# Optimization experiments

Hardware: AMD Instinct MI355X
Metric: run time of the kernel (lower is better)

The kernel has to match this reference:

```python
import jax, jax.numpy as jnp
import numpy as np

N = 50000
E = 800000
IN_DIM = 128
HID = 128
OUT = 40


def setup_inputs() -> dict:
    key = jax.random.key(0)
    k1, k2, k3, k4, k5 = jax.random.split(key, 5)
    x = jax.random.normal(k1, (N, IN_DIM), dtype=jnp.float32)
    edge_index = jax.random.randint(k2, (2, E), 0, N, dtype=jnp.int64)
    # Glorot-ish init for GCNConv weights, zero bias (PyG default bias=True)
    W1 = jax.random.normal(k3, (IN_DIM, HID), dtype=jnp.float32) / np.sqrt(IN_DIM)
    b1 = jnp.zeros((HID,), dtype=jnp.float32)
    W2 = jax.random.normal(k4, (HID, OUT), dtype=jnp.float32) / np.sqrt(HID)
    b2 = jnp.zeros((OUT,), dtype=jnp.float32)
    return {"x": x, "edge_index": edge_index, "W1": W1, "b1": b1, "W2": W2, "b2": b2}


def _gcn_norm(edge_index, n_nodes):
    """Add self-loops and compute symmetric GCN normalization per edge.
    Returns (src, dst, norm) with len E + n_nodes."""
    loops = jnp.arange(n_nodes, dtype=edge_index.dtype)
    src = jnp.concatenate([edge_index[0], loops])
    dst = jnpp_concat = jnp.concatenate([edge_index[1], loops])
    dst = jnp.concatenate([edge_index[1], loops])
    deg = jax.ops.segment_sum(jnp.ones_like(dst, dtype=jnp.float32), dst,
                              num_segments=n_nodes)
    dinv = jnp.where(deg > 0, jax.lax.rsqrt(deg), 0.0)
    norm = dinv[src] * dinv[dst]  # [E + N]
    return src, dst, norm


def _gcn_conv(x, src, dst, norm, W, b, n_nodes):
    xw = x @ W                                  # [N, F_out] transform first
    msg = xw[src] * norm[:, None]               # gather + scale, [E+N, F_out]
    out = jax.ops.segment_sum(msg, dst, num_segments=n_nodes)  # scatter-add
    return out + b


def reference(x, edge_index, W1, b1, W2, b2):
    n = x.shape[0]
    src, dst, norm = _gcn_norm(edge_index, n)
    h = _gcn_conv(x, src, dst, norm, W1, b1, n)
    h = jax.nn.relu(h)
    # dropout is identity in eval mode (training=False)
    h = _gcn_conv(h, src, dst, norm, W2, b2, n)
    return jax.nn.softmax(h, axis=1)
```

## Files before the change

### kernel.cpp

```cpp
#include <hip/hip_runtime.h>
#include <hip/hip_fp16.h>

#define IN_DIM 128
#define HID    128
#define OUTC   40
#define CAP    64
#define LSTR   136
#define NBS    1024
#define NBG1   256

typedef _Float16 f16x8 __attribute__((ext_vector_type(8)));
typedef _Float16 f16x4 __attribute__((ext_vector_type(4)));
typedef float    f32x4 __attribute__((ext_vector_type(4)));
typedef int      i32x4 __attribute__((ext_vector_type(4)));

__device__ __forceinline__ int permi(int d, int NP8) { return (d & 7) * NP8 + (d >> 3); }

__device__ __forceinline__ f16x8 cvt8(f32x4 lo, f32x4 hi) {
  f16x8 r;
  r[0] = (_Float16)lo[0]; r[1] = (_Float16)lo[1]; r[2] = (_Float16)lo[2]; r[3] = (_Float16)lo[3];
  r[4] = (_Float16)hi[0]; r[5] = (_Float16)hi[1]; r[6] = (_Float16)hi[2]; r[7] = (_Float16)hi[3];
  return r;
}

__global__ __launch_bounds__(256) void k_scatter_gemm1(const int* __restrict__ edge, int* __restrict__ cnt,
                                                       unsigned short* __restrict__ col,
                                                       const float* __restrict__ x, const float* __restrict__ W1,
                                                       __half* __restrict__ xws,
                                                       int E, int n, int NP8, int nT) {
  __shared__ _Float16 sW[128 * 128];
  int b   = blockIdx.x;
  int c40 = b / 40, r40 = b % 40;
  int tid = threadIdx.x;
  int E4  = E >> 2;

  if (r40 < 32) {
    int g = b & 7;
    auto proc = [&](int d, int s) {
      if ((d & 7) != g || (unsigned)d >= (unsigned)n || (unsigned)s >= (unsigned)n) return;
      int p   = g * NP8 + (d >> 3);
      int pos = atomicAdd(&cnt[p], 1);
      if (pos < CAP) col[(size_t)p * CAP + pos] = (unsigned short)s;
    };
    int j = c40 * 4 + (r40 >> 3);
    int t = j * 256 + tid;
    const int gstride = (NBS >> 3) * 256;
    const i32x4* srcv = (const i32x4*)edge;
    const i32x4* dstv = (const i32x4*)&edge[E];
    for (int q = t; q < E4; q += gstride) {
      i32x4 dq = __builtin_nontemporal_load(&dstv[q]);
      i32x4 sq = __builtin_nontemporal_load(&srcv[q]);
      proc(dq[0], sq[0]); proc(dq[1], sq[1]); proc(dq[2], sq[2]); proc(dq[3], sq[3]);
    }
    if (b == 0) {
      for (int e = E4 * 4 + tid; e < E; e += 256) {
        int d  = edge[E + e];
        int sv = edge[e];
        if ((unsigned)d >= (unsigned)n || (unsigned)sv >= (unsigned)n) continue;
        int p   = (d & 7) * NP8 + (d >> 3);
        int pos = atomicAdd(&cnt[p], 1);
        if (pos < CAP) col[(size_t)p * CAP + pos] = (unsigned short)sv;
      }
    }
    return;
  }

  {
    const f32x4* w4 = (const f32x4*)W1;
    for (int idx = tid; idx < 4096; idx += 256) {
      int kk = idx >> 5, nn4 = (idx & 31) * 4;
      f32x4 v = w4[idx];
#pragma unroll
      for (int j = 0; j < 4; ++j) {
        int nn = nn4 + j;
        sW[nn * 128 + (kk ^ ((nn & 7) << 3))] = (_Float16)v[j];
      }
    }
  }
  __syncthreads();
  int wv = tid >> 6, lane = tid & 63, m = lane & 15, quad = lane >> 4;
  int sw = (m & 7) << 3;
  int bg = c40 * 8 + (r40 - 32);
  for (int tile = bg; tile < nT; tile += NBG1) {
    int i0   = tile * 64;
    int arow = i0 + 16 * wv + m;
    f16x8 a0, a1, a2, a3;
    if (arow < n) {
      const float* xr = &x[(size_t)arow * IN_DIM + quad * 8];
      f32x4 u0 = __builtin_nontemporal_load((const f32x4*)(xr));
      f32x4 u1 = __builtin_nontemporal_load((const f32x4*)(xr + 4));
      f32x4 u2 = __builtin_nontemporal_load((const f32x4*)(xr + 32));
      f32x4 u3 = __builtin_nontemporal_load((const f32x4*)(xr + 36));
      f32x4 u4 = __builtin_nontemporal_load((const f32x4*)(xr + 64));
      f32x4 u5 = __builtin_nontemporal_load((const f32x4*)(xr + 68));
      f32x4 u6 = __builtin_nontemporal_load((const f32x4*)(xr + 96));
      f32x4 u7 = __builtin_nontemporal_load((const f32x4*)(xr + 100));
      a0 = cvt8(u0, u1); a1 = cvt8(u2, u3); a2 = cvt8(u4, u5); a3 = cvt8(u6, u7);
    } else {
#pragma unroll
      for (int jj = 0; jj < 8; ++jj) {
        a0[jj] = (_Float16)0.f; a1[jj] = (_Float16)0.f; a2[jj] = (_Float16)0.f; a3[jj] = (_Float16)0.f;
      }
    }
    int base_row = i0 + 16 * wv + quad * 4;
#pragma unroll
    for (int t = 0; t < 8; ++t) {
      const _Float16* bx = &sW[(t * 16 + m) * 128];
      f16x8 bf0 = *(const f16x8*)&bx[(quad * 8 +  0) ^ sw];
      f16x8 bf1 = *(const f16x8*)&bx[(quad * 8 + 32) ^ sw];
      f16x8 bf2 = *(const f16x8*)&bx[(quad * 8 + 64) ^ sw];
      f16x8 bf3 = *(const f16x8*)&bx[(quad * 8 + 96) ^ sw];
      f32x4 c = {0.f, 0.f, 0.f, 0.f};
      c = __builtin_amdgcn_mfma_f32_16x16x32_f16(a0, bf0, c, 0, 0, 0);
      c = __builtin_amdgcn_mfma_f32_16x16x32_f16(a1, bf1, c, 0, 0, 0);
      c = __builtin_amdgcn_mfma_f32_16x16x32_f16(a2, bf2, c, 0, 0, 0);
      c = __builtin_amdgcn_mfma_f32_16x16x32_f16(a3, bf3, c, 0, 0, 0);
      int colb = t * 16 + m;
#pragma unroll
      for (int r = 0; r < 4; ++r) {
        int row = base_row + r;
        if (row < n) xws[(size_t)row * HID + colb] = __float2half(c[r]);
      }
    }
  }
}

__global__ __launch_bounds__(256) void k_agg1(const uint2* __restrict__ xws2, const int* __restrict__ cnt,
                                              const unsigned short* __restrict__ col, const float* __restrict__ b1,
                                              uint2* __restrict__ hv, int n, int NP8) {
  int wvid = (blockIdx.x * 256 + threadIdx.x) >> 6;
  int lane = threadIdx.x & 63;
  int half = lane >> 5;
  int f    = lane & 31;
  int wid  = wvid * 2 + half;
  if (wid >= n) return;
  int p   = permi(wid, NP8);
  int deg = cnt[p];
  float dvd = rsqrtf((float)(deg + 1));
  uint2 sv = xws2[(size_t)wid * 32 + f];
  float2 slo = __half22float2(*(__half2*)&sv.x);
  float2 shi = __half22float2(*(__half2*)&sv.y);
  float ax = slo.x * dvd, ay = slo.y * dvd, az = shi.x * dvd, aw = shi.y * dvd;
  int end = min(deg, CAP);
  const unsigned short* cp = &col[(size_t)p * CAP];
  int e = 0;
  for (; e + 4 <= end; e += 4) {
    uint2 cw = *(const uint2*)&cp[e];
    int s0 = cw.x & 0xffff, s1 = cw.x >> 16;
    int s2 = cw.y & 0xffff, s3 = cw.y >> 16;
    float d0 = rsqrtf((float)(cnt[permi(s0, NP8)] + 1));
    float d1 = rsqrtf((float)(cnt[permi(s1, NP8)] + 1));
    float d2 = rsqrtf((float)(cnt[permi(s2, NP8)] + 1));
    float d3 = rsqrtf((float)(cnt[permi(s3, NP8)] + 1));
    uint2 v0 = xws2[(size_t)s0 * 32 + f];
    uint2 v1 = xws2[(size_t)s1 * 32 + f];
    uint2 v2 = xws2[(size_t)s2 * 32 + f];
    uint2 v3 = xws2[(size_t)s3 * 32 + f];
    float2 l0 = __half22float2(*(__half2*)&v0.x), h0 = __half22float2(*(__half2*)&v0.y);
    float2 l1 = __half22float2(*(__half2*)&v1.x), h1 = __half22float2(*(__half2*)&v1.y);
    float2 l2 = __half22float2(*(__half2*)&v2.x), h2 = __half22float2(*(__half2*)&v2.y);
    float2 l3 = __half22float2(*(__half2*)&v3.x), h3 = __half22float2(*(__half2*)&v3.y);
    ax += l0.x * d0 + l1.x * d1 + l2.x * d2 + l3.x * d3;
    ay += l0.y * d0 + l1.y * d1 + l2.y * d2 + l3.y * d3;
    az += h0.x * d0 + h1.x * d1 + h2.x * d2 + h3.x * d3;
    aw += h0.y * d0 + h1.y * d1 + h2.y * d2 + h3.y * d3;
  }
  for (; e < end; ++e) {
    int s    = cp[e];
    float dv = rsqrtf((float)(cnt[permi(s, NP8)] + 1));
    uint2 v  = xws2[(size_t)s * 32 + f];
    float2 l = __half22float2(*(__half2*)&v.x), hh = __half22float2(*(__half2*)&v.y);
    ax += l.x * dv; ay += l.y * dv; az += hh.x * dv; aw += hh.y * dv;
  }
  float4 bb = ((const float4*)b1)[f];
  __half2 o0 = __floats2half2_rn(fmaxf(ax * dvd + bb.x, 0.f), fmaxf(ay * dvd + bb.y, 0.f));
  __half2 o1 = __floats2half2_rn(fmaxf(az * dvd + bb.z, 0.f), fmaxf(aw * dvd + bb.w, 0.f));
  uint2 o; o.x = *(unsigned*)&o0; o.y = *(unsigned*)&o1;
  hv[(size_t)wid * 32 + f] = o;
}

__global__ __launch_bounds__(256) void k_gemm2(const __half* __restrict__ h, const float* __restrict__ W2,
                                               const int* __restrict__ cnt, __half* __restrict__ out,
                                               int n, int NP8) {
  __shared__ _Float16 sW[48 * LSTR];
  __shared__ _Float16 sH[64 * LSTR];
  int tid = threadIdx.x;
  int i0  = blockIdx.x * 64;

  for (int idx = tid; idx < 8192; idx += 256) {
    int nn = idx & 63, kk = idx >> 6;
    if (nn < 48) sW[nn * LSTR + kk] = (nn < OUTC) ? (_Float16)W2[kk * OUTC + nn] : (_Float16)0.f;
  }
  {
    const uint4* src = (const uint4*)h;
    for (int idx = tid; idx < 1024; idx += 256) {
      int r = idx >> 4, c = idx & 15;
      int row = i0 + r;
      uint4 v = (row < n) ? src[(size_t)row * 16 + c] : make_uint4(0u, 0u, 0u, 0u);
      *(uint4*)&sH[r * LSTR + c * 8] = v;
    }
  }
  __syncthreads();

  int wv = tid >> 6, lane = tid & 63, m = lane & 15, quad = lane >> 4;
  const _Float16* axp = &sH[(16 * wv + m) * LSTR + quad * 8];
  f16x8 a0 = *(const f16x8*)(axp);
  f16x8 a1 = *(const f16x8*)(axp + 32);
  f16x8 a2 = *(const f16x8*)(axp + 64);
  f16x8 a3 = *(const f16x8*)(axp + 96);

  int base_row = i0 + 16 * wv + quad * 4;
  float dvr[4];
#pragma unroll
  for (int r = 0; r < 4; ++r) {
    int row = base_row + r;
    dvr[r] = (row < n) ? rsqrtf((float)(cnt[permi(row, NP8)] + 1)) : 0.f;
  }

#pragma unroll
  for (int t = 0; t < 3; ++t) {
    const _Float16* bx = &sW[(t * 16 + m) * LSTR + quad * 8];
    f16x8 bf0 = *(const f16x8*)(bx);
    f16x8 bf1 = *(const f16x8*)(bx + 32);
    f16x8 bf2 = *(const f16x8*)(bx + 64);
    f16x8 bf3 = *(const f16x8*)(bx + 96);
    f32x4 c = {0.f, 0.f, 0.f, 0.f};
    c = __builtin_amdgcn_mfma_f32_16x16x32_f16(a0, bf0, c, 0, 0, 0);
    c = __builtin_amdgcn_mfma_f32_16x16x32_f16(a1, bf1, c, 0, 0, 0);
    c = __builtin_amdgcn_mfma_f32_16x16x32_f16(a2, bf2, c, 0, 0, 0);
    c = __builtin_amdgcn_mfma_f32_16x16x32_f16(a3, bf3, c, 0, 0, 0);
    int colb = t * 16 + m;
    if (colb < OUTC) {
#pragma unroll
      for (int r = 0; r < 4; ++r) {
        int row = base_row + r;
        if (row < n) out[(size_t)row * OUTC + colb] = __float2half(c[r] * dvr[r]);
      }
    }
  }
}

__global__ __launch_bounds__(256) void k_agg2(const __half2* __restrict__ hw2, const int* __restrict__ cnt,
                                              const unsigned short* __restrict__ col, const float* __restrict__ b2,
                                              float* __restrict__ out, int n, int NP8) {
  int wpair = (blockIdx.x * 256 + threadIdx.x) >> 6;
  int lane  = threadIdx.x & 63;
  int half  = lane >> 5;
  int f     = lane & 31;
  int wid   = wpair * 2 + half;
  bool act  = (f < OUTC / 2) && (wid < n);
  int widc  = (wid < n) ? wid : 0;
  int li    = act ? f : 0;
  int p     = permi(widc, NP8);
  int deg   = (wid < n) ? cnt[p] : 0;
  float2 acc = act ? __half22float2(hw2[(size_t)widc * (OUTC / 2) + li]) : make_float2(0.f, 0.f);
  int end = min(deg, CAP);
  const unsigned short* cp = &col[(size_t)p * CAP];
  int e = 0;
  for (; e + 8 <= end; e += 8) {
    uint4 cw = *(const uint4*)&cp[e];
    int s0 = cw.x & 0xffff, s1 = cw.x >> 16, s2 = cw.y & 0xffff, s3 = cw.y >> 16;
    int s4 = cw.z & 0xffff, s5 = cw.z >> 16, s6 = cw.w & 0xffff, s7 = cw.w >> 16;
    if (act) {
      float2 v0 = __half22float2(hw2[(size_t)s0 * (OUTC / 2) + li]);
      float2 v1 = __half22float2(hw2[(size_t)s1 * (OUTC / 2) + li]);
      float2 v2 = __half22float2(hw2[(size_t)s2 * (OUTC / 2) + li]);
      float2 v3 = __half22float2(hw2[(size_t)s3 * (OUTC / 2) + li]);
      float2 v4 = __half22float2(hw2[(size_t)s4 * (OUTC / 2) + li]);
      float2 v5 = __half22float2(hw2[(size_t)s5 * (OUTC / 2) + li]);
      float2 v6 = __half22float2(hw2[(size_t)s6 * (OUTC / 2) + li]);
      float2 v7 = __half22float2(hw2[(size_t)s7 * (OUTC / 2) + li]);
      acc.x += (v0.x + v1.x) + (v2.x + v3.x) + ((v4.x + v5.x) + (v6.x + v7.x));
      acc.y += (v0.y + v1.y) + (v2.y + v3.y) + ((v4.y + v5.y) + (v6.y + v7.y));
    }
  }
  for (; e < end; ++e) {
    int s = cp[e];
    if (act) {
      float2 v = __half22float2(hw2[(size_t)s * (OUTC / 2) + li]);
      acc.x += v.x; acc.y += v.y;
    }
  }
  float dvd = rsqrtf((float)(deg + 1));
  float2 bb = act ? ((const float2*)b2)[li] : make_float2(0.f, 0.f);
  float lx = act ? acc.x * dvd + bb.x : -1e30f;
  float ly = act ? acc.y * dvd + bb.y : -1e30f;
  float m = fmaxf(lx, ly);
#pragma unroll
  for (int o = 16; o > 0; o >>= 1) m = fmaxf(m, __shfl_xor(m, o, 32));
  float ex = act ? __expf(lx - m) : 0.f;
  float ey = act ? __expf(ly - m) : 0.f;
  float sum = ex + ey;
#pragma unroll
  for (int o = 16; o > 0; o >>= 1) sum += __shfl_xor(sum, o, 32);
  if (act) {
    float inv = 1.f / sum;
    ((float2*)out)[(size_t)wid * (OUTC / 2) + li] = make_float2(ex * inv, ey * inv);
  }
}


extern "C" void kernel_launch(void* const* d_in, const int* in_sizes, int n_in,
                              void* d_out, int out_size, void* d_ws, size_t ws_size,
                              hipStream_t stream) {
  const float* x    = (const float*)d_in[0];
  const int*   edge = (const int*)d_in[1];
  const float* W1   = (const float*)d_in[2];
  const float* b1   = (const float*)d_in[3];
  const float* W2   = (const float*)d_in[4];
  const float* b2   = (const float*)d_in[5];
  float* out = (float*)d_out;

  int N   = in_sizes[0] / IN_DIM;
  int E   = in_sizes[1] / 2;
  int NP8 = (N + 7) / 8;
  int NP  = NP8 * 8;

  char* ws = (char*)d_ws;
  size_t off = 0;
  auto carve = [&](size_t bytes) { char* p = ws + off; off = (off + bytes + 255) & ~(size_t)255; return p; };
  int*            cnt = (int*)carve((size_t)NP * 4);
  unsigned short* col = (unsigned short*)carve((size_t)NP * CAP * 2);
  __half*         xws = (__half*)carve((size_t)N * HID * 2);
  __half*         h   = (__half*)carve((size_t)N * HID * 2);
  __half*         hw  = xws;

  (void)hipMemsetAsync(cnt, 0, (size_t)NP * 4, stream);

  int nT  = (N + 63) / 64;
  int nbA = ((N + 1) / 2 * 64 + 255) / 256;

  k_scatter_gemm1<<<NBS + NBG1, 256, 0, stream>>>(edge, cnt, col, x, W1, xws, E, N, NP8, nT);
  k_agg1<<<nbA, 256, 0, stream>>>((const uint2*)xws, cnt, col, b1, (uint2*)h, N, NP8);
  k_gemm2<<<nT, 256, 0, stream>>>(h, W2, cnt, hw, N, NP8);
  k_agg2<<<nbA, 256, 0, stream>>>((const __half2*)hw, cnt, col, b2, out, N, NP8);
}
```

Measured before the change: 212.6 us.

## Split scatter from GEMM1 and fold source-degree scaling into GEMM1 output

Breaks the fused scatter+GEMM1 kernel into two kernels so GEMM1 can read the finished degree counts and pre-scale each row of XW by its rsqrt(deg+1). This removes the per-edge degree lookups and rsqrt calls from the layer-1 aggregation. The aggregation is also split into two feature halves, with 16 lanes per node, to change its gather access pattern and the number of blocks. GEMM1 now uses a padded LDS layout instead of the XOR swizzle. The cost is an extra kernel launch and the loss of the overlap between scatter and GEMM1.

```diff
diff --git a/kernel.cpp b/kernel.cpp
--- a/kernel.cpp
+++ b/kernel.cpp
@@ -7,7 +7,6 @@
 #define CAP    64
 #define LSTR   136
 #define NBS    1024
-#define NBG1   256
 
 typedef _Float16 f16x8 __attribute__((ext_vector_type(8)));
 typedef _Float16 f16x4 __attribute__((ext_vector_type(4)));
@@ -23,124 +22,128 @@
   return r;
 }
 
-__global__ __launch_bounds__(256) void k_scatter_gemm1(const int* __restrict__ edge, int* __restrict__ cnt,
-                                                       unsigned short* __restrict__ col,
-                                                       const float* __restrict__ x, const float* __restrict__ W1,
-                                                       __half* __restrict__ xws,
-                                                       int E, int n, int NP8, int nT) {
-  __shared__ _Float16 sW[128 * 128];
-  int b   = blockIdx.x;
-  int c40 = b / 40, r40 = b % 40;
+__global__ __launch_bounds__(256) void k_scatter(const int* __restrict__ edge, int* __restrict__ cnt,
+                                                 unsigned short* __restrict__ col,
+                                                 int E, int n, int NP8) {
+  int b = blockIdx.x, tid = threadIdx.x;
+  int g = b & 7;
+  int E4 = E >> 2;
+  auto proc = [&](int d, int s) {
+    if ((d & 7) != g || (unsigned)d >= (unsigned)n || (unsigned)s >= (unsigned)n) return;
+    int p   = g * NP8 + (d >> 3);
+    int pos = atomicAdd(&cnt[p], 1);
+    if (pos < CAP) col[(size_t)p * CAP + pos] = (unsigned short)s;
+  };
+  int j = b >> 3;
+  int t = j * 256 + tid;
+  const int gstride = (NBS >> 3) * 256;
+  const i32x4* srcv = (const i32x4*)edge;
+  const i32x4* dstv = (const i32x4*)&edge[E];
+  for (int q = t; q < E4; q += gstride) {
+    i32x4 dq = __builtin_nontemporal_load(&dstv[q]);
+    i32x4 sq = __builtin_nontemporal_load(&srcv[q]);
+    proc(dq[0], sq[0]); proc(dq[1], sq[1]); proc(dq[2], sq[2]); proc(dq[3], sq[3]);
+  }
+  if (b == 0) {
+    for (int e = E4 * 4 + tid; e < E; e += 256) {
+      int d  = edge[E + e];
+      int sv = edge[e];
+      if ((unsigned)d >= (unsigned)n || (unsigned)sv >= (unsigned)n) continue;
+      int p   = (d & 7) * NP8 + (d >> 3);
+      int pos = atomicAdd(&cnt[p], 1);
+      if (pos < CAP) col[(size_t)p * CAP + pos] = (unsigned short)sv;
+    }
+  }
+}
+
+__global__ __launch_bounds__(256) void k_gemm1(const float* __restrict__ x, const float* __restrict__ W1,
+                                               const int* __restrict__ cnt, __half* __restrict__ xws,
+                                               int n, int NP8) {
+  __shared__ _Float16 sW[128 * LSTR];
   int tid = threadIdx.x;
-  int E4  = E >> 2;
-
-  if (r40 < 32) {
-    int g = b & 7;
-    auto proc = [&](int d, int s) {
-      if ((d & 7) != g || (unsigned)d >= (unsigned)n || (unsigned)s >= (unsigned)n) return;
-      int p   = g * NP8 + (d >> 3);
-      int pos = atomicAdd(&cnt[p], 1);
-      if (pos < CAP) col[(size_t)p * CAP + pos] = (unsigned short)s;
-    };
-    int j = c40 * 4 + (r40 >> 3);
-    int t = j * 256 + tid;
-    const int gstride = (NBS >> 3) * 256;
-    const i32x4* srcv = (const i32x4*)edge;
-    const i32x4* dstv = (const i32x4*)&edge[E];
-    for (int q = t; q < E4; q += gstride) {
-      i32x4 dq = __builtin_nontemporal_load(&dstv[q]);
-      i32x4 sq = __builtin_nontemporal_load(&srcv[q]);
-      proc(dq[0], sq[0]); proc(dq[1], sq[1]); proc(dq[2], sq[2]); proc(dq[3], sq[3]);
-    }
-    if (b == 0) {
-      for (int e = E4 * 4 + tid; e < E; e += 256) {
-        int d  = edge[E + e];
-        int sv = edge[e];
-        if ((unsigned)d >= (unsigned)n || (unsigned)sv >= (unsigned)n) continue;
-        int p   = (d & 7) * NP8 + (d >> 3);
-        int pos = atomicAdd(&cnt[p], 1);
-        if (pos < CAP) col[(size_t)p * CAP + pos] = (unsigned short)sv;
-      }
-    }
-    return;
-  }
+  int i0  = blockIdx.x * 64;
 
   {
     const f32x4* w4 = (const f32x4*)W1;
     for (int idx = tid; idx < 4096; idx += 256) {
       int kk = idx >> 5, nn4 = (idx & 31) * 4;
       f32x4 v = w4[idx];
-#pragma unroll
-      for (int j = 0; j < 4; ++j) {
-        int nn = nn4 + j;
-        sW[nn * 128 + (kk ^ ((nn & 7) << 3))] = (_Float16)v[j];
-      }
+      sW[(nn4 + 0) * LSTR + kk] = (_Float16)v[0];
+      sW[(nn4 + 1) * LSTR + kk] = (_Float16)v[1];
+      sW[(nn4 + 2) * LSTR + kk] = (_Float16)v[2];
+      sW[(nn4 + 3) * LSTR + kk] = (_Float16)v[3];
     }
   }
   __syncthreads();
+
   int wv = tid >> 6, lane = tid & 63, m = lane & 15, quad = lane >> 4;
-  int sw = (m & 7) << 3;
-  int bg = c40 * 8 + (r40 - 32);
-  for (int tile = bg; tile < nT; tile += NBG1) {
-    int i0   = tile * 64;
-    int arow = i0 + 16 * wv + m;
-    f16x8 a0, a1, a2, a3;
-    if (arow < n) {
-      const float* xr = &x[(size_t)arow * IN_DIM + quad * 8];
-      f32x4 u0 = __builtin_nontemporal_load((const f32x4*)(xr));
-      f32x4 u1 = __builtin_nontemporal_load((const f32x4*)(xr + 4));
-      f32x4 u2 = __builtin_nontemporal_load((const f32x4*)(xr + 32));
-      f32x4 u3 = __builtin_nontemporal_load((const f32x4*)(xr + 36));
-      f32x4 u4 = __builtin_nontemporal_load((const f32x4*)(xr + 64));
-      f32x4 u5 = __builtin_nontemporal_load((const f32x4*)(xr + 68));
-      f32x4 u6 = __builtin_nontemporal_load((const f32x4*)(xr + 96));
-      f32x4 u7 = __builtin_nontemporal_load((const f32x4*)(xr + 100));
-      a0 = cvt8(u0, u1); a1 = cvt8(u2, u3); a2 = cvt8(u4, u5); a3 = cvt8(u6, u7);
-    } else {
-#pragma unroll
-      for (int jj = 0; jj < 8; ++jj) {
-        a0[jj] = (_Float16)0.f; a1[jj] = (_Float16)0.f; a2[jj] = (_Float16)0.f; a3[jj] = (_Float16)0.f;
-      }
-    }
-    int base_row = i0 + 16 * wv + quad * 4;
-#pragma unroll
-    for (int t = 0; t < 8; ++t) {
-      const _Float16* bx = &sW[(t * 16 + m) * 128];
-      f16x8 bf0 = *(const f16x8*)&bx[(quad * 8 +  0) ^ sw];
-      f16x8 bf1 = *(const f16x8*)&bx[(quad * 8 + 32) ^ sw];
-      f16x8 bf2 = *(const f16x8*)&bx[(quad * 8 + 64) ^ sw];
-      f16x8 bf3 = *(const f16x8*)&bx[(quad * 8 + 96) ^ sw];
-      f32x4 c = {0.f, 0.f, 0.f, 0.f};
-      c = __builtin_amdgcn_mfma_f32_16x16x32_f16(a0, bf0, c, 0, 0, 0);
-      c = __builtin_amdgcn_mfma_f32_16x16x32_f16(a1, bf1, c, 0, 0, 0);
-      c = __builtin_amdgcn_mfma_f32_16x16x32_f16(a2, bf2, c, 0, 0, 0);
-      c = __builtin_amdgcn_mfma_f32_16x16x32_f16(a3, bf3, c, 0, 0, 0);
-      int colb = t * 16 + m;
-#pragma unroll
-      for (int r = 0; r < 4; ++r) {
-        int row = base_row + r;
-        if (row < n) xws[(size_t)row * HID + colb] = __float2half(c[r]);
-      }
+  int arow = i0 + 16 * wv + m;
+  f16x8 a0, a1, a2, a3;
+  if (arow < n) {
+    const float* xr = &x[(size_t)arow * IN_DIM + quad * 8];
+    f32x4 u0 = __builtin_nontemporal_load((const f32x4*)(xr));
+    f32x4 u1 = __builtin_nontemporal_load((const f32x4*)(xr + 4));
+    f32x4 u2 = __builtin_nontemporal_load((const f32x4*)(xr + 32));
+    f32x4 u3 = __builtin_nontemporal_load((const f32x4*)(xr + 36));
+    f32x4 u4 = __builtin_nontemporal_load((const f32x4*)(xr + 64));
+    f32x4 u5 = __builtin_nontemporal_load((const f32x4*)(xr + 68));
+    f32x4 u6 = __builtin_nontemporal_load((const f32x4*)(xr + 96));
+    f32x4 u7 = __builtin_nontemporal_load((const f32x4*)(xr + 100));
+    a0 = cvt8(u0, u1); a1 = cvt8(u2, u3); a2 = cvt8(u4, u5); a3 = cvt8(u6, u7);
+  } else {
+#pragma unroll
+    for (int jj = 0; jj < 8; ++jj) {
+      a0[jj] = (_Float16)0.f; a1[jj] = (_Float16)0.f; a2[jj] = (_Float16)0.f; a3[jj] = (_Float16)0.f;
+    }
+  }
+
+  int base_row = i0 + 16 * wv + quad * 4;
+  float dvr[4];
+#pragma unroll
+  for (int r = 0; r < 4; ++r) {
+    int row = base_row + r;
+    dvr[r] = (row < n) ? rsqrtf((float)(cnt[permi(row, NP8)] + 1)) : 0.f;
+  }
+
+#pragma unroll
+  for (int t = 0; t < 8; ++t) {
+    const _Float16* bx = &sW[(t * 16 + m) * LSTR + quad * 8];
+    f16x8 bf0 = *(const f16x8*)(bx);
+    f16x8 bf1 = *(const f16x8*)(bx + 32);
+    f16x8 bf2 = *(const f16x8*)(bx + 64);
+    f16x8 bf3 = *(const f16x8*)(bx + 96);
+    f32x4 c = {0.f, 0.f, 0.f, 0.f};
+    c = __builtin_amdgcn_mfma_f32_16x16x32_f16(a0, bf0, c, 0, 0, 0);
+    c = __builtin_amdgcn_mfma_f32_16x16x32_f16(a1, bf1, c, 0, 0, 0);
+    c = __builtin_amdgcn_mfma_f32_16x16x32_f16(a2, bf2, c, 0, 0, 0);
+    c = __builtin_amdgcn_mfma_f32_16x16x32_f16(a3, bf3, c, 0, 0, 0);
+    int colb = t * 16 + m;
+#pragma unroll
+    for (int r = 0; r < 4; ++r) {
+      int row = base_row + r;
+      if (row < n) xws[(size_t)row * HID + colb] = __float2half(c[r] * dvr[r]);
     }
   }
 }
 
 __global__ __launch_bounds__(256) void k_agg1(const uint2* __restrict__ xws2, const int* __restrict__ cnt,
                                               const unsigned short* __restrict__ col, const float* __restrict__ b1,
-                                              uint2* __restrict__ hv, int n, int NP8) {
-  int wvid = (blockIdx.x * 256 + threadIdx.x) >> 6;
-  int lane = threadIdx.x & 63;
-  int half = lane >> 5;
-  int f    = lane & 31;
-  int wid  = wvid * 2 + half;
+                                              uint2* __restrict__ hv, int n, int NP8, int nbHalf) {
+  int bi = blockIdx.x, tid = threadIdx.x;
+  int ph = 0;
+  if (bi >= nbHalf) { ph = 1; bi -= nbHalf; }
+  int sub = (tid >> 4) & 3;
+  int f16i = tid & 15;
+  int wid = bi * 16 + ((tid >> 6) << 2) + sub;
   if (wid >= n) return;
+  int fo = ph * 16 + f16i;
   int p   = permi(wid, NP8);
   int deg = cnt[p];
   float dvd = rsqrtf((float)(deg + 1));
-  uint2 sv = xws2[(size_t)wid * 32 + f];
-  float2 slo = __half22float2(*(__half2*)&sv.x);
-  float2 shi = __half22float2(*(__half2*)&sv.y);
-  float ax = slo.x * dvd, ay = slo.y * dvd, az = shi.x * dvd, aw = shi.y * dvd;
+  uint2 sv = xws2[(size_t)wid * 32 + fo];
+  float2 alo = __half22float2(*(__half2*)&sv.x);
+  float2 ahi = __half22float2(*(__half2*)&sv.y);
+  float ax = alo.x, ay = alo.y, az = ahi.x, aw = ahi.y;
   int end = min(deg, CAP);
   const unsigned short* cp = &col[(size_t)p * CAP];
   int e = 0;
@@ -148,35 +151,29 @@
     uint2 cw = *(const uint2*)&cp[e];
     int s0 = cw.x & 0xffff, s1 = cw.x >> 16;
     int s2 = cw.y & 0xffff, s3 = cw.y >> 16;
-    float d0 = rsqrtf((float)(cnt[permi(s0, NP8)] + 1));
-    float d1 = rsqrtf((float)(cnt[permi(s1, NP8)] + 1));
-    float d2 = rsqrtf((float)(cnt[permi(s2, NP8)] + 1));
-    float d3 = rsqrtf((float)(cnt[permi(s3, NP8)] + 1));
-    uint2 v0 = xws2[(size_t)s0 * 32 + f];
-    uint2 v1 = xws2[(size_t)s1 * 32 + f];
-    uint2 v2 = xws2[(size_t)s2 * 32 + f];
-    uint2 v3 = xws2[(size_t)s3 * 32 + f];
+    uint2 v0 = xws2[(size_t)s0 * 32 + fo];
+    uint2 v1 = xws2[(size_t)s1 * 32 + fo];
+    uint2 v2 = xws2[(size_t)s2 * 32 + fo];
+    uint2 v3 = xws2[(size_t)s3 * 32 + fo];
     float2 l0 = __half22float2(*(__half2*)&v0.x), h0 = __half22float2(*(__half2*)&v0.y);
     float2 l1 = __half22float2(*(__half2*)&v1.x), h1 = __half22float2(*(__half2*)&v1.y);
     float2 l2 = __half22float2(*(__half2*)&v2.x), h2 = __half22float2(*(__half2*)&v2.y);
     float2 l3 = __half22float2(*(__half2*)&v3.x), h3 = __half22float2(*(__half2*)&v3.y);
-    ax += l0.x * d0 + l1.x * d1 + l2.x * d2 + l3.x * d3;
-    ay += l0.y * d0 + l1.y * d1 + l2.y * d2 + l3.y * d3;
-    az += h0.x * d0 + h1.x * d1 + h2.x * d2 + h3.x * d3;
-    aw += h0.y * d0 + h1.y * d1 + h2.y * d2 + h3.y * d3;
+    ax += (l0.x + l1.x) + (l2.x + l3.x);
+    ay += (l0.y + l1.y) + (l2.y + l3.y);
+    az += (h0.x + h1.x) + (h2.x + h3.x);
+    aw += (h0.y + h1.y) + (h2.y + h3.y);
   }
   for (; e < end; ++e) {
-    int s    = cp[e];
-    float dv = rsqrtf((float)(cnt[permi(s, NP8)] + 1));
-    uint2 v  = xws2[(size_t)s * 32 + f];
+    uint2 v = xws2[(size_t)cp[e] * 32 + fo];
     float2 l = __half22float2(*(__half2*)&v.x), hh = __half22float2(*(__half2*)&v.y);
-    ax += l.x * dv; ay += l.y * dv; az += hh.x * dv; aw += hh.y * dv;
-  }
-  float4 bb = ((const float4*)b1)[f];
+    ax += l.x; ay += l.y; az += hh.x; aw += hh.y;
+  }
+  float4 bb = ((const float4*)b1)[fo];
   __half2 o0 = __floats2half2_rn(fmaxf(ax * dvd + bb.x, 0.f), fmaxf(ay * dvd + bb.y, 0.f));
   __half2 o1 = __floats2half2_rn(fmaxf(az * dvd + bb.z, 0.f), fmaxf(aw * dvd + bb.w, 0.f));
   uint2 o; o.x = *(unsigned*)&o0; o.y = *(unsigned*)&o1;
-  hv[(size_t)wid * 32 + f] = o;
+  hv[(size_t)wid * 32 + fo] = o;
 }
 
 __global__ __launch_bounds__(256) void k_gemm2(const __half* __restrict__ h, const float* __restrict__ W2,
@@ -327,11 +324,13 @@
 
   (void)hipMemsetAsync(cnt, 0, (size_t)NP * 4, stream);
 
-  int nT  = (N + 63) / 64;
-  int nbA = ((N + 1) / 2 * 64 + 255) / 256;
-
-  k_scatter_gemm1<<<NBS + NBG1, 256, 0, stream>>>(edge, cnt, col, x, W1, xws, E, N, NP8, nT);
-  k_agg1<<<nbA, 256, 0, stream>>>((const uint2*)xws, cnt, col, b1, (uint2*)h, N, NP8);
+  int nT     = (N + 63) / 64;
+  int nbHalf = (N + 15) / 16;
+  int nbA2   = ((N + 1) / 2 * 64 + 255) / 256;
+
+  k_scatter<<<NBS, 256, 0, stream>>>(edge, cnt, col, E, N, NP8);
+  k_gemm1<<<nT, 256, 0, stream>>>(x, W1, cnt, xws, N, NP8);
+  k_agg1<<<2 * nbHalf, 256, 0, stream>>>((const uint2*)xws, cnt, col, b1, (uint2*)h, N, NP8, nbHalf);
   k_gemm2<<<nT, 256, 0, stream>>>(h, W2, cnt, hw, N, NP8);
-  k_agg2<<<nbA, 256, 0, stream>>>((const __half2*)hw, cnt, col, b2, out, N, NP8);
-}
+  k_agg2<<<nbA2, 256, 0, stream>>>((const __half2*)hw, cnt, col, b2, out, N, NP8);
+}
```

After: 217.8 us. 2.4% more time.
